# Kernel tuning notes

Hardware: AMD Instinct MI355X
Metric: run time of the kernel (lower is better)

The kernel has to match this reference:

```python
import math
import jax, jax.numpy as jnp
import numpy as np

SIN_DIM = 8
HEADS = 4
HID = 64
EMBED = 6 + 1 + 3 * SIN_DIM + 5 + 2  # 38


def _sinusoidal(v):
    # v: [N] -> [N, SIN_DIM], interleaved sin/cos as in torch.stack(...).flatten(-2)
    div = jnp.exp(jnp.arange(0, SIN_DIM, 2, dtype=jnp.float32) * (-math.log(10000.0) / SIN_DIM))
    scaled = v[:, None] * div  # [N, SIN_DIM//2]
    return jnp.stack([jnp.sin(scaled), jnp.cos(scaled)], axis=-1).reshape(v.shape[0], SIN_DIM)


def _feature_embed(x):
    nt = jnp.clip(x[:, 0].astype(jnp.int32), 0, 5)
    role = jnp.clip(x[:, 5].astype(jnp.int32), 0, 4)
    return jnp.concatenate([
        jax.nn.one_hot(nt, 6, dtype=x.dtype),
        jnp.log1p(x[:, 1])[:, None],
        _sinusoidal(x[:, 2]),
        _sinusoidal(x[:, 3]),
        _sinusoidal(x[:, 4] * 100.0),
        jax.nn.one_hot(role, 5, dtype=x.dtype),
        x[:, 6:7],
        x[:, 7:8],
    ], axis=-1)  # [N, 38]


def _gat(x, adj, W, a_src, a_dst, concat):
    N = x.shape[0]
    h = (x @ W).reshape(N, HEADS, HID)                       # [N,H,D]
    src = jnp.einsum('nhd,hd->nh', h, a_src)                 # [N,H]
    dst = jnp.einsum('nhd,hd->nh', h, a_dst)                 # [N,H]
    e = src[:, None, :] + dst[None, :, :]                    # [N,N,H]
    e = jnp.where(e > 0, e, 0.2 * e)                         # leaky_relu(0.2)
    e = jnp.where(adj[:, :, None] > 0, e, -jnp.inf)
    a = jax.nn.softmax(e, axis=1)                            # softmax over neighbors j
    out = jnp.einsum('njh,nhd->nhd'.replace('nj', 'ij').replace('nhd,', 'jhd,').replace('->nhd', '->ihd'), a, h) if False else jnp.einsum('ijh,jhd->ihd', a, h)
    if concat:
        return out.reshape(N, HEADS * HID)
    return out.mean(axis=1)


def _layernorm(x, g, b, eps=1e-5):
    mu = x.mean(axis=-1, keepdims=True)
    var = ((x - mu) ** 2).mean(axis=-1, keepdims=True)
    return (x - mu) / jnp.sqrt(var + eps) * g + b


def setup_inputs() -> dict:
    key = jax.random.key(0)
    ks = jax.random.split(key, 16)
    N, C = 4096, 512
    # raw node features per FeatureEmbedding docstring
    nt = jax.random.randint(ks[0], (N,), 0, 6).astype(jnp.float32)
    arity = jax.random.randint(ks[1], (N,), 0, 5).astype(jnp.float32)
    arg_pos = jax.random.randint(ks[2], (N,), 0, 8).astype(jnp.float32)
    depth = jax.random.randint(ks[3], (N,), 0, 12).astype(jnp.float32)
    age = jax.random.uniform(ks[4], (N,))
    role = jax.random.randint(ks[5], (N,), 0, 5).astype(jnp.float32)
    pol = jax.random.bernoulli(ks[6], 0.5, (N,)).astype(jnp.float32)
    eq = jax.random.bernoulli(ks[7], 0.2, (N,)).astype(jnp.float32)
    node_features = jnp.stack([nt, arity, arg_pos, depth, age, role, pol, eq], axis=-1)
    adj = (jax.random.uniform(ks[8], (N, N)) < 0.01).astype(jnp.float32)
    adj = jnp.maximum(adj, jnp.eye(N, dtype=jnp.float32))  # self-loops
    pm = (jax.random.uniform(ks[9], (C, N)) < (8.0 / N)).astype(jnp.float32)
    pool_matrix = pm / jnp.clip(pm.sum(axis=1, keepdims=True), 1.0, None)
    def xavier(k, shape):
        fan = shape[0] + shape[-1]
        return jax.random.normal(k, shape, dtype=jnp.float32) * math.sqrt(2.0 / fan)
    return {
        'node_features': node_features, 'adj': adj, 'pool_matrix': pool_matrix,
        'W1': xavier(ks[10], (EMBED, HID * HEADS)),
        'a_src1': xavier(ks[11], (HEADS, HID)), 'a_dst1': xavier(ks[12], (HEADS, HID)),
        'g1': jnp.ones((HID * HEADS,), jnp.float32), 'b1': jnp.zeros((HID * HEADS,), jnp.float32),
        'W2': xavier(ks[13], (HID * HEADS, HID * HEADS)),
        'a_src2': xavier(ks[14], (HEADS, HID)), 'a_dst2': xavier(ks[15], (HEADS, HID)),
        'g2': jnp.ones((HID,), jnp.float32), 'b2': jnp.zeros((HID,), jnp.float32),
        'Ws': xavier(jax.random.fold_in(key, 100), (HID, HID)), 'bs': jnp.zeros((HID,), jnp.float32),
        'Wo': xavier(jax.random.fold_in(key, 101), (HID, 1)), 'bo': jnp.zeros((1,), jnp.float32),
    }


def reference(node_features, adj, pool_matrix, W1, a_src1, a_dst1, g1, b1,
              W2, a_src2, a_dst2, g2, b2, Ws, bs, Wo, bo):
    x = _feature_embed(node_features)                         # [N, 38]
    # layer 1: concat heads -> [N, 256]
    x = jax.nn.elu(_layernorm(_gat(x, adj, W1, a_src1, a_dst1, True), g1, b1))
    # layer 2: mean over heads -> [N, 64]  (dropout is eval-mode no-op)
    x = jax.nn.elu(_layernorm(_gat(x, adj, W2, a_src2, a_dst2, False), g2, b2))
    clause_emb = pool_matrix @ x                               # [C, 64]
    h = jax.nn.relu(clause_emb @ Ws + bs)                      # MLP scorer
    return (h @ Wo + bo)[:, 0]                                 # [C]
```

## Files before the change

### kernel.cpp

```cpp
#include <hip/hip_runtime.h>
#include <math.h>

#define N 4096
#define C 512
#define EMB 38
#define HEADS 4
#define HID 64
#define F1 256
#define MAXN 128
#define R2 8

__device__ __forceinline__ float wr_sum(float v) {
#pragma unroll
    for (int o = 32; o > 0; o >>= 1) v += __shfl_xor(v, o);
    return v;
}
__device__ __forceinline__ float wr_max(float v) {
#pragma unroll
    for (int o = 32; o > 0; o >>= 1) v = fmaxf(v, __shfl_xor(v, o));
    return v;
}

__global__ __launch_bounds__(256) void k_build(const float* __restrict__ adj,
                                               int* __restrict__ cnt, int* __restrict__ idx) {
    int wv = threadIdx.x >> 6, lane = threadIdx.x & 63;
    int i = blockIdx.x * 4 + wv;
    const float4* row = (const float4*)(adj + (size_t)i * N);
    unsigned long long below = (lane == 63) ? ~0ull >> 1 : (1ull << lane) - 1;
    int base = 0;
    int* orow = idx + i * MAXN;
#pragma unroll 2
    for (int it = 0; it < 16; ++it) {
        float4 a = row[it * 64 + lane];
        int col0 = 4 * (it * 64 + lane);
        float vals[4] = {a.x, a.y, a.z, a.w};
#pragma unroll
        for (int comp = 0; comp < 4; ++comp) {
            unsigned long long m = __ballot(vals[comp] > 0.f);
            if (vals[comp] > 0.f) {
                int p = base + __popcll(m & below);
                if (p < MAXN) orow[p] = col0 + comp;
            }
            base += __popcll(m);
        }
    }
    if (lane == 0) cnt[i] = min(base, MAXN);
}

__global__ __launch_bounds__(256) void k_gemm1(const float* __restrict__ nf, const float* __restrict__ W1,
                                               const float* __restrict__ asrc, const float* __restrict__ adst,
                                               float* __restrict__ h1, float* __restrict__ s1, float* __restrict__ d1) {
    int n0 = blockIdx.x * R2, tid = threadIdx.x;
    __shared__ float fs[R2][8];
    __shared__ float xs[R2][40];
    if (tid < R2 * 8) fs[tid >> 3][tid & 7] = nf[(size_t)(n0 + (tid >> 3)) * 8 + (tid & 7)];
    if (tid < R2 * 2) xs[tid >> 1][38 + (tid & 1)] = 0.f;
    __syncthreads();
    {
        int r = tid & 7;
        int t = tid >> 3;
        const float* f = fs[r];
        for (int pass = 0; pass < 2; ++pass, t += 32) {
            if (t >= EMB) break;
            float val;
            if (t < 6) { int nt = min(max((int)f[0], 0), 5); val = (t == nt) ? 1.f : 0.f; }
            else if (t == 6) val = log1pf(f[1]);
            else if (t < 31) {
                int q = (t - 7) & 7, s = (t - 7) >> 3, m = q >> 1;
                float base = (s == 0) ? f[2] : (s == 1) ? f[3] : f[4] * 100.f;
                float div = expf((2.f * m) * (-logf(10000.f) / 8.f));
                float sc = base * div;
                val = (q & 1) ? cosf(sc) : sinf(sc);
            }
            else if (t < 36) { int role = min(max((int)f[5], 0), 4); val = (t - 31 == role) ? 1.f : 0.f; }
            else val = (t == 36) ? f[6] : f[7];
            xs[r][t] = val;
        }
    }
    __syncthreads();
    float acc[R2];
#pragma unroll
    for (int r = 0; r < R2; ++r) acc[r] = 0.f;
#pragma unroll
    for (int kk = 0; kk < 9; ++kk) {
        float w0 = W1[(4 * kk + 0) * F1 + tid];
        float w1 = W1[(4 * kk + 1) * F1 + tid];
        float w2 = W1[(4 * kk + 2) * F1 + tid];
        float w3 = W1[(4 * kk + 3) * F1 + tid];
#pragma unroll
        for (int r = 0; r < R2; ++r) {
            float4 x = *(const float4*)&xs[r][4 * kk];
            acc[r] = fmaf(x.x, w0, fmaf(x.y, w1, fmaf(x.z, w2, fmaf(x.w, w3, acc[r]))));
        }
    }
#pragma unroll
    for (int k = 36; k < EMB; ++k) {
        float wv = W1[k * F1 + tid];
#pragma unroll
        for (int r = 0; r < R2; ++r) acc[r] = fmaf(xs[r][k], wv, acc[r]);
    }
    int h = tid >> 6, lane = tid & 63;
    float av = asrc[tid], dv = adst[tid];
#pragma unroll
    for (int r = 0; r < R2; ++r) {
        h1[(size_t)(n0 + r) * F1 + tid] = acc[r];
        float ss = wr_sum(acc[r] * av);
        float dd = wr_sum(acc[r] * dv);
        if (lane == 0) { s1[(n0 + r) * HEADS + h] = ss; d1[(n0 + r) * HEADS + h] = dd; }
    }
}

__global__ __launch_bounds__(256) void k_gemm2(const float* __restrict__ x1, const float* __restrict__ W2,
                                               const float* __restrict__ asrc, const float* __restrict__ adst,
                                               float* __restrict__ h2, float* __restrict__ s2, float* __restrict__ d2) {
    int n0 = blockIdx.x * R2, tid = threadIdx.x;
    __shared__ float4 xs4[R2][F1 / 4];
    {
        int r = tid >> 5, kk = tid & 31;
        const float4* x1v = (const float4*)x1;
        xs4[r][kk]      = x1v[(size_t)(n0 + r) * 64 + kk];
        xs4[r][kk + 32] = x1v[(size_t)(n0 + r) * 64 + kk + 32];
    }
    __syncthreads();
    float acc[R2];
#pragma unroll
    for (int r = 0; r < R2; ++r) acc[r] = 0.f;
    for (int kk = 0; kk < F1 / 4; ++kk) {
        float w0 = W2[(4 * kk + 0) * F1 + tid];
        float w1 = W2[(4 * kk + 1) * F1 + tid];
        float w2 = W2[(4 * kk + 2) * F1 + tid];
        float w3 = W2[(4 * kk + 3) * F1 + tid];
#pragma unroll
        for (int r = 0; r < R2; ++r) {
            float4 x = xs4[r][kk];
            acc[r] = fmaf(x.x, w0, fmaf(x.y, w1, fmaf(x.z, w2, fmaf(x.w, w3, acc[r]))));
        }
    }
    int h = tid >> 6, lane = tid & 63;
    float av = asrc[tid], dv = adst[tid];
#pragma unroll
    for (int r = 0; r < R2; ++r) {
        h2[(size_t)(n0 + r) * F1 + tid] = acc[r];
        float ss = wr_sum(acc[r] * av);
        float dd = wr_sum(acc[r] * dv);
        if (lane == 0) { s2[(n0 + r) * HEADS + h] = ss; d2[(n0 + r) * HEADS + h] = dd; }
    }
}

__global__ __launch_bounds__(256) void k_agg1(const float* __restrict__ h1, const float* __restrict__ s1,
                                              const float* __restrict__ d1, const int* __restrict__ cnt,
                                              const int* __restrict__ idx, const float* __restrict__ g,
                                              const float* __restrict__ b, float* __restrict__ xo) {
    int i = blockIdx.x, tid = threadIdx.x;
    int wv = tid >> 6, lane = tid & 63;
    __shared__ int nbrs[MAXN];
    __shared__ float wts[HEADS][MAXN + 1];
    __shared__ float lsum[HEADS];
    __shared__ float sacc[4][F1];
    __shared__ float red[HEADS];
    int c = cnt[i];
    if (tid < c) nbrs[tid] = idx[i * MAXN + tid];
    __syncthreads();
    if (tid < c) {
        float4 dd = ((const float4*)d1)[nbrs[tid]];
        float4 ss = ((const float4*)s1)[i];
        float e0 = ss.x + dd.x, e1 = ss.y + dd.y, e2 = ss.z + dd.z, e3 = ss.w + dd.w;
        wts[0][tid] = e0 > 0.f ? e0 : 0.2f * e0;
        wts[1][tid] = e1 > 0.f ? e1 : 0.2f * e1;
        wts[2][tid] = e2 > 0.f ? e2 : 0.2f * e2;
        wts[3][tid] = e3 > 0.f ? e3 : 0.2f * e3;
    }
    __syncthreads();
    {
        float m = -INFINITY;
        for (int jj = lane; jj < c; jj += 64) m = fmaxf(m, wts[wv][jj]);
        m = wr_max(m);
        float l = 0.f;
        for (int jj = lane; jj < c; jj += 64) { float t = expf(wts[wv][jj] - m); wts[wv][jj] = t; l += t; }
        l = wr_sum(l);
        if (lane == 0) lsum[wv] = l;
    }
    __syncthreads();
    int hq = lane >> 4;
    const float4* hv = (const float4*)h1;
    float4 acc = {0.f, 0.f, 0.f, 0.f};
    int jj = wv;
    for (; jj + 4 < c; jj += 8) {
        int na = nbrs[jj], nb = nbrs[jj + 4];
        float wa = wts[hq][jj], wb = wts[hq][jj + 4];
        float4 va = hv[(size_t)na * 64 + lane];
        float4 vb = hv[(size_t)nb * 64 + lane];
        acc.x = fmaf(wa, va.x, acc.x); acc.y = fmaf(wa, va.y, acc.y);
        acc.z = fmaf(wa, va.z, acc.z); acc.w = fmaf(wa, va.w, acc.w);
        acc.x = fmaf(wb, vb.x, acc.x); acc.y = fmaf(wb, vb.y, acc.y);
        acc.z = fmaf(wb, vb.z, acc.z); acc.w = fmaf(wb, vb.w, acc.w);
    }
    for (; jj < c; jj += 4) {
        int na = nbrs[jj];
        float wa = wts[hq][jj];
        float4 va = hv[(size_t)na * 64 + lane];
        acc.x = fmaf(wa, va.x, acc.x); acc.y = fmaf(wa, va.y, acc.y);
        acc.z = fmaf(wa, va.z, acc.z); acc.w = fmaf(wa, va.w, acc.w);
    }
    ((float4*)&sacc[wv][0])[lane] = acc;
    __syncthreads();
    int h = tid >> 6;
    float tot = (sacc[0][tid] + sacc[1][tid] + sacc[2][tid] + sacc[3][tid]) / lsum[h];
    float s = wr_sum(tot);
    if (lane == 0) red[h] = s;
    __syncthreads();
    float mu = (red[0] + red[1] + red[2] + red[3]) * (1.f / F1);
    float dvv = tot - mu;
    float s2 = wr_sum(dvv * dvv);
    __syncthreads();
    if (lane == 0) red[h] = s2;
    __syncthreads();
    float var = (red[0] + red[1] + red[2] + red[3]) * (1.f / F1);
    float y = dvv * rsqrtf(var + 1e-5f) * g[tid] + b[tid];
    xo[(size_t)i * F1 + tid] = y > 0.f ? y : expm1f(y);
}

__global__ __launch_bounds__(256) void k_agg2(const float* __restrict__ h2, const float* __restrict__ s2,
                                              const float* __restrict__ d2, const int* __restrict__ cnt,
                                              const int* __restrict__ idx, const float* __restrict__ g,
                                              const float* __restrict__ b, float* __restrict__ xo) {
    int i = blockIdx.x, tid = threadIdx.x;
    int wv = tid >> 6, lane = tid & 63;
    __shared__ int nbrs[MAXN];
    __shared__ float wts[HEADS][MAXN + 1];
    __shared__ float lsum[HEADS];
    __shared__ float sacc[4][F1];
    int c = cnt[i];
    if (tid < c) nbrs[tid] = idx[i * MAXN + tid];
    __syncthreads();
    if (tid < c) {
        float4 dd = ((const float4*)d2)[nbrs[tid]];
        float4 ss = ((const float4*)s2)[i];
        float e0 = ss.x + dd.x, e1 = ss.y + dd.y, e2 = ss.z + dd.z, e3 = ss.w + dd.w;
        wts[0][tid] = e0 > 0.f ? e0 : 0.2f * e0;
        wts[1][tid] = e1 > 0.f ? e1 : 0.2f * e1;
        wts[2][tid] = e2 > 0.f ? e2 : 0.2f * e2;
        wts[3][tid] = e3 > 0.f ? e3 : 0.2f * e3;
    }
    __syncthreads();
    {
        float m = -INFINITY;
        for (int jj = lane; jj < c; jj += 64) m = fmaxf(m, wts[wv][jj]);
        m = wr_max(m);
        float l = 0.f;
        for (int jj = lane; jj < c; jj += 64) { float t = expf(wts[wv][jj] - m); wts[wv][jj] = t; l += t; }
        l = wr_sum(l);
        if (lane == 0) lsum[wv] = l;
    }
    __syncthreads();
    int hq = lane >> 4;
    const float4* hvv = (const float4*)h2;
    float4 acc = {0.f, 0.f, 0.f, 0.f};
    int jj = wv;
    for (; jj + 4 < c; jj += 8) {
        int na = nbrs[jj], nb = nbrs[jj + 4];
        float wa = wts[hq][jj], wb = wts[hq][jj + 4];
        float4 va = hvv[(size_t)na * 64 + lane];
        float4 vb = hvv[(size_t)nb * 64 + lane];
        acc.x = fmaf(wa, va.x, acc.x); acc.y = fmaf(wa, va.y, acc.y);
        acc.z = fmaf(wa, va.z, acc.z); acc.w = fmaf(wa, va.w, acc.w);
        acc.x = fmaf(wb, vb.x, acc.x); acc.y = fmaf(wb, vb.y, acc.y);
        acc.z = fmaf(wb, vb.z, acc.z); acc.w = fmaf(wb, vb.w, acc.w);
    }
    for (; jj < c; jj += 4) {
        int na = nbrs[jj];
        float wa = wts[hq][jj];
        float4 va = hvv[(size_t)na * 64 + lane];
        acc.x = fmaf(wa, va.x, acc.x); acc.y = fmaf(wa, va.y, acc.y);
        acc.z = fmaf(wa, va.z, acc.z); acc.w = fmaf(wa, va.w, acc.w);
    }
    ((float4*)&sacc[wv][0])[lane] = acc;
    __syncthreads();
    if (wv == 0) {
        float t0 = 0.f, t1 = 0.f, t2 = 0.f, t3 = 0.f;
#pragma unroll
        for (int w = 0; w < 4; ++w) {
            t0 += sacc[w][lane];
            t1 += sacc[w][lane + 64];
            t2 += sacc[w][lane + 128];
            t3 += sacc[w][lane + 192];
        }
        float mv = (t0 / lsum[0] + t1 / lsum[1] + t2 / lsum[2] + t3 / lsum[3]) * 0.25f;
        float mu = wr_sum(mv) * (1.f / HID);
        float dvv = mv - mu;
        float var = wr_sum(dvv * dvv) * (1.f / HID);
        float y = dvv * rsqrtf(var + 1e-5f) * g[lane] + b[lane];
        xo[i * HID + lane] = y > 0.f ? y : expm1f(y);
    }
}

__global__ __launch_bounds__(256) void k_poolscore(const float* __restrict__ pm, const float* __restrict__ x2,
                                                   const float* __restrict__ Ws, const float* __restrict__ bs,
                                                   const float* __restrict__ Wo, const float* __restrict__ bo,
                                                   float* __restrict__ out) {
    int c = blockIdx.x, tid = threadIdx.x;
    int w = tid >> 6, lane = tid & 63;
    __shared__ float sacc[4][HID];
    __shared__ float ce_s[HID];
    float acc = 0.f;
    const float4* pmv = (const float4*)(pm + (size_t)c * N);
#pragma unroll
    for (int it = 0; it < 4; ++it) {
        int vi = w * 256 + it * 64 + lane;
        float4 p4 = pmv[vi];
        float pc[4] = {p4.x, p4.y, p4.z, p4.w};
#pragma unroll
        for (int comp = 0; comp < 4; ++comp) {
            unsigned long long msk = __ballot(pc[comp] != 0.f);
            while (msk) {
                int bpos = __ffsll(msk) - 1;
                msk &= msk - 1;
                float pj = __shfl(pc[comp], bpos);
                int j = (w * 256 + it * 64 + bpos) * 4 + comp;
                acc += pj * x2[(size_t)j * HID + lane];
            }
        }
    }
    sacc[w][lane] = acc;
    __syncthreads();
    if (w == 0) {
        ce_s[lane] = sacc[0][lane] + sacc[1][lane] + sacc[2][lane] + sacc[3][lane];
    }
    __syncthreads();
    if (w == 0) {
        float hd = bs[lane];
#pragma unroll 8
        for (int k = 0; k < HID; ++k) hd = fmaf(ce_s[k], Ws[k * HID + lane], hd);
        hd = fmaxf(hd, 0.f);
        float v = wr_sum(hd * Wo[lane]);
        if (lane == 0) out[c] = v + bo[0];
    }
}

extern "C" void kernel_launch(void* const* d_in, const int* in_sizes, int n_in,
                              void* d_out, int out_size, void* d_ws, size_t ws_size,
                              hipStream_t stream) {
    const float* nf  = (const float*)d_in[0];
    const float* adj = (const float*)d_in[1];
    const float* pm  = (const float*)d_in[2];
    const float* W1  = (const float*)d_in[3];
    const float* as1 = (const float*)d_in[4];
    const float* ad1 = (const float*)d_in[5];
    const float* g1  = (const float*)d_in[6];
    const float* b1  = (const float*)d_in[7];
    const float* W2  = (const float*)d_in[8];
    const float* as2 = (const float*)d_in[9];
    const float* ad2 = (const float*)d_in[10];
    const float* g2  = (const float*)d_in[11];
    const float* b2  = (const float*)d_in[12];
    const float* Ws  = (const float*)d_in[13];
    const float* bs  = (const float*)d_in[14];
    const float* Wo  = (const float*)d_in[15];
    const float* bo  = (const float*)d_in[16];
    float* out = (float*)d_out;

    float* p = (float*)d_ws;
    float* h1  = p; p += (size_t)N * F1;
    float* s1  = p; p += (size_t)N * HEADS;
    float* d1  = p; p += (size_t)N * HEADS;
    float* x1  = p; p += (size_t)N * F1;
    float* h2  = p; p += (size_t)N * F1;
    float* s2  = p; p += (size_t)N * HEADS;
    float* d2  = p; p += (size_t)N * HEADS;
    float* x2  = p; p += (size_t)N * HID;
    int* cnt = (int*)p;
    int* idx = cnt + N;

    k_build<<<N / 4, 256, 0, stream>>>(adj, cnt, idx);
    k_gemm1<<<N / R2, 256, 0, stream>>>(nf, W1, as1, ad1, h1, s1, d1);
    k_agg1<<<N, 256, 0, stream>>>(h1, s1, d1, cnt, idx, g1, b1, x1);
    k_gemm2<<<N / R2, 256, 0, stream>>>(x1, W2, as2, ad2, h2, s2, d2);
    k_agg2<<<N, 256, 0, stream>>>(h2, s2, d2, cnt, idx, g2, b2, x2);
    k_poolscore<<<C, 256, 0, stream>>>(pm, x2, Ws, bs, Wo, bo, out);
}
```

Baseline: 201.5 us.

## Fuse all GAT stages into one cooperative persistent kernel with grid syncs

Replaces the six separate launches with a single cooperative kernel of 512 blocks that runs adjacency compaction, both GEMMs, both aggregations and pooling/scoring, separated by grid-wide barriers. Each block handles 8 rows per stage, and shared memory is reused across stages through a union. The aim is to remove per-kernel launch and drain overhead. In exchange, the aggregation stages drop from 4096 blocks to 512 blocks looping serially, which may reduce latency hiding, and the grid syncs add their own cost. The old multi-kernel path is kept as a fallback if the cooperative launch fails.

```diff
diff --git a/kernel.cpp b/kernel.cpp
--- a/kernel.cpp
+++ b/kernel.cpp
@@ -1,5 +1,8 @@
 #include <hip/hip_runtime.h>
+#include <hip/hip_cooperative_groups.h>
 #include <math.h>
+
+namespace cg = cooperative_groups;
 
 #define N 4096
 #define C 512
@@ -8,7 +11,8 @@
 #define HID 64
 #define F1 256
 #define MAXN 128
-#define R2 8
+#define RPB 8
+#define BLKS 512
 
 __device__ __forceinline__ float wr_sum(float v) {
 #pragma unroll
@@ -21,7 +25,344 @@
     return v;
 }
 
-__global__ __launch_bounds__(256) void k_build(const float* __restrict__ adj,
+struct SmemAgg {
+    int nbrs[MAXN];
+    float wts[HEADS][MAXN + 1];
+    float lsum[HEADS];
+    float sacc[4][F1];
+    float red[HEADS];
+};
+struct SmemG1 {
+    float fs[RPB][8];
+    float xs[RPB][40];
+};
+struct SmemG2 {
+    float4 xs4[RPB][F1 / 4];
+};
+struct SmemPool {
+    float sacc[4][HID];
+    float ce[HID];
+};
+union Smem {
+    SmemAgg a;
+    SmemG1 g1;
+    SmemG2 g2;
+    SmemPool p;
+};
+
+__global__ __launch_bounds__(256, 2) void k_all(
+        const float* __restrict__ adj, const float* __restrict__ nf, const float* __restrict__ pm,
+        const float* __restrict__ W1, const float* __restrict__ as1, const float* __restrict__ ad1,
+        const float* __restrict__ g1, const float* __restrict__ b1,
+        const float* __restrict__ W2, const float* __restrict__ as2, const float* __restrict__ ad2,
+        const float* __restrict__ g2, const float* __restrict__ b2,
+        const float* __restrict__ Wsc, const float* __restrict__ bsc,
+        const float* __restrict__ Wo, const float* __restrict__ bo,
+        float* __restrict__ out, float* __restrict__ ws) {
+    cg::grid_group gg = cg::this_grid();
+    __shared__ Smem sm;
+    int tid = threadIdx.x, blk = blockIdx.x;
+    int wv = tid >> 6, lane = tid & 63;
+
+    float* h1 = ws;
+    float* s1 = h1 + (size_t)N * F1;
+    float* d1 = s1 + N * HEADS;
+    float* x1 = d1 + N * HEADS;
+    float* h2 = x1 + (size_t)N * F1;
+    float* s2 = h2 + (size_t)N * F1;
+    float* d2 = s2 + N * HEADS;
+    float* x2 = d2 + N * HEADS;
+    int* cnt  = (int*)(x2 + N * HID);
+    int* idx  = cnt + N;
+
+#pragma unroll
+    for (int rep = 0; rep < 2; ++rep) {
+        int i = blk * RPB + rep * 4 + wv;
+        const float4* row = (const float4*)(adj + (size_t)i * N);
+        unsigned long long below = (lane == 63) ? (~0ull >> 1) : ((1ull << lane) - 1);
+        int base = 0;
+        int* orow = idx + i * MAXN;
+        for (int it = 0; it < 16; ++it) {
+            float4 a = row[it * 64 + lane];
+            int col0 = 4 * (it * 64 + lane);
+            float vals[4] = {a.x, a.y, a.z, a.w};
+#pragma unroll
+            for (int comp = 0; comp < 4; ++comp) {
+                unsigned long long m = __ballot(vals[comp] > 0.f);
+                if (vals[comp] > 0.f) {
+                    int p = base + __popcll(m & below);
+                    if (p < MAXN) orow[p] = col0 + comp;
+                }
+                base += __popcll(m);
+            }
+        }
+        if (lane == 0) cnt[i] = min(base, MAXN);
+    }
+
+    {
+        int n0 = blk * RPB;
+        if (tid < RPB * 8) sm.g1.fs[tid >> 3][tid & 7] = nf[(size_t)n0 * 8 + tid];
+        if (tid < RPB * 2) sm.g1.xs[tid >> 1][38 + (tid & 1)] = 0.f;
+        __syncthreads();
+        {
+            int r = tid & 7;
+            int t = tid >> 3;
+            const float* f = sm.g1.fs[r];
+            for (int pass = 0; pass < 2; ++pass, t += 32) {
+                if (t >= EMB) break;
+                float val;
+                if (t < 6) { int nt = min(max((int)f[0], 0), 5); val = (t == nt) ? 1.f : 0.f; }
+                else if (t == 6) val = log1pf(f[1]);
+                else if (t < 31) {
+                    int q = (t - 7) & 7, s = (t - 7) >> 3, m = q >> 1;
+                    float base = (s == 0) ? f[2] : (s == 1) ? f[3] : f[4] * 100.f;
+                    float div = expf((2.f * m) * (-logf(10000.f) / 8.f));
+                    float sc = base * div;
+                    val = (q & 1) ? cosf(sc) : sinf(sc);
+                }
+                else if (t < 36) { int role = min(max((int)f[5], 0), 4); val = (t - 31 == role) ? 1.f : 0.f; }
+                else val = (t == 36) ? f[6] : f[7];
+                sm.g1.xs[r][t] = val;
+            }
+        }
+        __syncthreads();
+        float acc[RPB];
+#pragma unroll
+        for (int r = 0; r < RPB; ++r) acc[r] = 0.f;
+#pragma unroll
+        for (int kk = 0; kk < 9; ++kk) {
+            float w0 = W1[(4 * kk + 0) * F1 + tid];
+            float w1 = W1[(4 * kk + 1) * F1 + tid];
+            float w2 = W1[(4 * kk + 2) * F1 + tid];
+            float w3 = W1[(4 * kk + 3) * F1 + tid];
+#pragma unroll
+            for (int r = 0; r < RPB; ++r) {
+                float4 x = *(const float4*)&sm.g1.xs[r][4 * kk];
+                acc[r] = fmaf(x.x, w0, fmaf(x.y, w1, fmaf(x.z, w2, fmaf(x.w, w3, acc[r]))));
+            }
+        }
+#pragma unroll
+        for (int k = 36; k < EMB; ++k) {
+            float wvv = W1[k * F1 + tid];
+#pragma unroll
+            for (int r = 0; r < RPB; ++r) acc[r] = fmaf(sm.g1.xs[r][k], wvv, acc[r]);
+        }
+        float av = as1[tid], dvv = ad1[tid];
+#pragma unroll
+        for (int r = 0; r < RPB; ++r) {
+            h1[(size_t)(n0 + r) * F1 + tid] = acc[r];
+            float ssum = wr_sum(acc[r] * av);
+            float dsum = wr_sum(acc[r] * dvv);
+            if (lane == 0) { s1[(n0 + r) * HEADS + wv] = ssum; d1[(n0 + r) * HEADS + wv] = dsum; }
+        }
+    }
+    gg.sync();
+
+    for (int rr = 0; rr < RPB; ++rr) {
+        int i = blk * RPB + rr;
+        __syncthreads();
+        int c = cnt[i];
+        if (tid < c) sm.a.nbrs[tid] = idx[i * MAXN + tid];
+        __syncthreads();
+        if (tid < c) {
+            float4 dd = ((const float4*)d1)[sm.a.nbrs[tid]];
+            float4 ss = ((const float4*)s1)[i];
+            float e0 = ss.x + dd.x, e1 = ss.y + dd.y, e2 = ss.z + dd.z, e3 = ss.w + dd.w;
+            sm.a.wts[0][tid] = e0 > 0.f ? e0 : 0.2f * e0;
+            sm.a.wts[1][tid] = e1 > 0.f ? e1 : 0.2f * e1;
+            sm.a.wts[2][tid] = e2 > 0.f ? e2 : 0.2f * e2;
+            sm.a.wts[3][tid] = e3 > 0.f ? e3 : 0.2f * e3;
+        }
+        __syncthreads();
+        {
+            float m = -INFINITY;
+            for (int jj = lane; jj < c; jj += 64) m = fmaxf(m, sm.a.wts[wv][jj]);
+            m = wr_max(m);
+            float l = 0.f;
+            for (int jj = lane; jj < c; jj += 64) { float t = expf(sm.a.wts[wv][jj] - m); sm.a.wts[wv][jj] = t; l += t; }
+            l = wr_sum(l);
+            if (lane == 0) sm.a.lsum[wv] = l;
+        }
+        __syncthreads();
+        int hq = lane >> 4;
+        const float4* hv = (const float4*)h1;
+        float4 acc = {0.f, 0.f, 0.f, 0.f};
+        int jj = wv;
+        for (; jj + 4 < c; jj += 8) {
+            int na = sm.a.nbrs[jj], nb = sm.a.nbrs[jj + 4];
+            float wa = sm.a.wts[hq][jj], wb = sm.a.wts[hq][jj + 4];
+            float4 va = hv[(size_t)na * 64 + lane];
+            float4 vb = hv[(size_t)nb * 64 + lane];
+            acc.x = fmaf(wa, va.x, acc.x); acc.y = fmaf(wa, va.y, acc.y);
+            acc.z = fmaf(wa, va.z, acc.z); acc.w = fmaf(wa, va.w, acc.w);
+            acc.x = fmaf(wb, vb.x, acc.x); acc.y = fmaf(wb, vb.y, acc.y);
+            acc.z = fmaf(wb, vb.z, acc.z); acc.w = fmaf(wb, vb.w, acc.w);
+        }
+        for (; jj < c; jj += 4) {
+            int na = sm.a.nbrs[jj];
+            float wa = sm.a.wts[hq][jj];
+            float4 va = hv[(size_t)na * 64 + lane];
+            acc.x = fmaf(wa, va.x, acc.x); acc.y = fmaf(wa, va.y, acc.y);
+            acc.z = fmaf(wa, va.z, acc.z); acc.w = fmaf(wa, va.w, acc.w);
+        }
+        ((float4*)&sm.a.sacc[wv][0])[lane] = acc;
+        __syncthreads();
+        float tot = (sm.a.sacc[0][tid] + sm.a.sacc[1][tid] + sm.a.sacc[2][tid] + sm.a.sacc[3][tid]) / sm.a.lsum[wv];
+        float s = wr_sum(tot);
+        if (lane == 0) sm.a.red[wv] = s;
+        __syncthreads();
+        float mu = (sm.a.red[0] + sm.a.red[1] + sm.a.red[2] + sm.a.red[3]) * (1.f / F1);
+        float dvv = tot - mu;
+        float s2v = wr_sum(dvv * dvv);
+        __syncthreads();
+        if (lane == 0) sm.a.red[wv] = s2v;
+        __syncthreads();
+        float var = (sm.a.red[0] + sm.a.red[1] + sm.a.red[2] + sm.a.red[3]) * (1.f / F1);
+        float y = dvv * rsqrtf(var + 1e-5f) * g1[tid] + b1[tid];
+        x1[(size_t)i * F1 + tid] = y > 0.f ? y : expm1f(y);
+    }
+
+    {
+        __syncthreads();
+        int n0 = blk * RPB;
+        {
+            int r = tid >> 5, kk = tid & 31;
+            const float4* x1v = (const float4*)x1;
+            sm.g2.xs4[r][kk]      = x1v[(size_t)(n0 + r) * 64 + kk];
+            sm.g2.xs4[r][kk + 32] = x1v[(size_t)(n0 + r) * 64 + kk + 32];
+        }
+        __syncthreads();
+        float acc[RPB];
+#pragma unroll
+        for (int r = 0; r < RPB; ++r) acc[r] = 0.f;
+        for (int kk = 0; kk < F1 / 4; ++kk) {
+            float w0 = W2[(4 * kk + 0) * F1 + tid];
+            float w1 = W2[(4 * kk + 1) * F1 + tid];
+            float w2 = W2[(4 * kk + 2) * F1 + tid];
+            float w3 = W2[(4 * kk + 3) * F1 + tid];
+#pragma unroll
+            for (int r = 0; r < RPB; ++r) {
+                float4 x = sm.g2.xs4[r][kk];
+                acc[r] = fmaf(x.x, w0, fmaf(x.y, w1, fmaf(x.z, w2, fmaf(x.w, w3, acc[r]))));
+            }
+        }
+        float av = as2[tid], dvv = ad2[tid];
+#pragma unroll
+        for (int r = 0; r < RPB; ++r) {
+            h2[(size_t)(n0 + r) * F1 + tid] = acc[r];
+            float ssum = wr_sum(acc[r] * av);
+            float dsum = wr_sum(acc[r] * dvv);
+            if (lane == 0) { s2[(n0 + r) * HEADS + wv] = ssum; d2[(n0 + r) * HEADS + wv] = dsum; }
+        }
+    }
+    gg.sync();
+
+    for (int rr = 0; rr < RPB; ++rr) {
+        int i = blk * RPB + rr;
+        __syncthreads();
+        int c = cnt[i];
+        if (tid < c) sm.a.nbrs[tid] = idx[i * MAXN + tid];
+        __syncthreads();
+        if (tid < c) {
+            float4 dd = ((const float4*)d2)[sm.a.nbrs[tid]];
+            float4 ss = ((const float4*)s2)[i];
+            float e0 = ss.x + dd.x, e1 = ss.y + dd.y, e2 = ss.z + dd.z, e3 = ss.w + dd.w;
+            sm.a.wts[0][tid] = e0 > 0.f ? e0 : 0.2f * e0;
+            sm.a.wts[1][tid] = e1 > 0.f ? e1 : 0.2f * e1;
+            sm.a.wts[2][tid] = e2 > 0.f ? e2 : 0.2f * e2;
+            sm.a.wts[3][tid] = e3 > 0.f ? e3 : 0.2f * e3;
+        }
+        __syncthreads();
+        {
+            float m = -INFINITY;
+            for (int jj = lane; jj < c; jj += 64) m = fmaxf(m, sm.a.wts[wv][jj]);
+            m = wr_max(m);
+            float l = 0.f;
+            for (int jj = lane; jj < c; jj += 64) { float t = expf(sm.a.wts[wv][jj] - m); sm.a.wts[wv][jj] = t; l += t; }
+            l = wr_sum(l);
+            if (lane == 0) sm.a.lsum[wv] = l;
+        }
+        __syncthreads();
+        int hq = lane >> 4;
+        const float4* hvv = (const float4*)h2;
+        float4 acc = {0.f, 0.f, 0.f, 0.f};
+        int jj = wv;
+        for (; jj + 4 < c; jj += 8) {
+            int na = sm.a.nbrs[jj], nb = sm.a.nbrs[jj + 4];
+            float wa = sm.a.wts[hq][jj], wb = sm.a.wts[hq][jj + 4];
+            float4 va = hvv[(size_t)na * 64 + lane];
+            float4 vb = hvv[(size_t)nb * 64 + lane];
+            acc.x = fmaf(wa, va.x, acc.x); acc.y = fmaf(wa, va.y, acc.y);
+            acc.z = fmaf(wa, va.z, acc.z); acc.w = fmaf(wa, va.w, acc.w);
+            acc.x = fmaf(wb, vb.x, acc.x); acc.y = fmaf(wb, vb.y, acc.y);
+            acc.z = fmaf(wb, vb.z, acc.z); acc.w = fmaf(wb, vb.w, acc.w);
+        }
+        for (; jj < c; jj += 4) {
+            int na = sm.a.nbrs[jj];
+            float wa = sm.a.wts[hq][jj];
+            float4 va = hvv[(size_t)na * 64 + lane];
+            acc.x = fmaf(wa, va.x, acc.x); acc.y = fmaf(wa, va.y, acc.y);
+            acc.z = fmaf(wa, va.z, acc.z); acc.w = fmaf(wa, va.w, acc.w);
+        }
+        ((float4*)&sm.a.sacc[wv][0])[lane] = acc;
+        __syncthreads();
+        if (wv == 0) {
+            float t0 = 0.f, t1 = 0.f, t2 = 0.f, t3 = 0.f;
+#pragma unroll
+            for (int w = 0; w < 4; ++w) {
+                t0 += sm.a.sacc[w][lane];
+                t1 += sm.a.sacc[w][lane + 64];
+                t2 += sm.a.sacc[w][lane + 128];
+                t3 += sm.a.sacc[w][lane + 192];
+            }
+            float mv = (t0 / sm.a.lsum[0] + t1 / sm.a.lsum[1] + t2 / sm.a.lsum[2] + t3 / sm.a.lsum[3]) * 0.25f;
+            float mu = wr_sum(mv) * (1.f / HID);
+            float dvv = mv - mu;
+            float var = wr_sum(dvv * dvv) * (1.f / HID);
+            float y = dvv * rsqrtf(var + 1e-5f) * g2[lane] + b2[lane];
+            x2[i * HID + lane] = y > 0.f ? y : expm1f(y);
+        }
+        __syncthreads();
+    }
+    gg.sync();
+
+    {
+        int cc = blk;
+        float acc = 0.f;
+        const float4* pmv = (const float4*)(pm + (size_t)cc * N);
+#pragma unroll
+        for (int it = 0; it < 4; ++it) {
+            int vi = wv * 256 + it * 64 + lane;
+            float4 p4 = pmv[vi];
+            float pc[4] = {p4.x, p4.y, p4.z, p4.w};
+#pragma unroll
+            for (int comp = 0; comp < 4; ++comp) {
+                unsigned long long msk = __ballot(pc[comp] != 0.f);
+                while (msk) {
+                    int bpos = __ffsll(msk) - 1;
+                    msk &= msk - 1;
+                    float pj = __shfl(pc[comp], bpos);
+                    int j = (wv * 256 + it * 64 + bpos) * 4 + comp;
+                    acc += pj * x2[(size_t)j * HID + lane];
+                }
+            }
+        }
+        sm.p.sacc[wv][lane] = acc;
+        __syncthreads();
+        if (wv == 0) sm.p.ce[lane] = sm.p.sacc[0][lane] + sm.p.sacc[1][lane] + sm.p.sacc[2][lane] + sm.p.sacc[3][lane];
+        __syncthreads();
+        if (wv == 0) {
+            float hd = bsc[lane];
+#pragma unroll 8
+            for (int k = 0; k < HID; ++k) hd = fmaf(sm.p.ce[k], Wsc[k * HID + lane], hd);
+            hd = fmaxf(hd, 0.f);
+            float v = wr_sum(hd * Wo[lane]);
+            if (lane == 0) out[cc] = v + bo[0];
+        }
+    }
+}
+
+__global__ __launch_bounds__(256) void f_build(const float* __restrict__ adj,
                                                int* __restrict__ cnt, int* __restrict__ idx) {
     int wv = threadIdx.x >> 6, lane = threadIdx.x & 63;
     int i = blockIdx.x * 4 + wv;
@@ -47,14 +388,14 @@
     if (lane == 0) cnt[i] = min(base, MAXN);
 }
 
-__global__ __launch_bounds__(256) void k_gemm1(const float* __restrict__ nf, const float* __restrict__ W1,
+__global__ __launch_bounds__(256) void f_gemm1(const float* __restrict__ nf, const float* __restrict__ W1,
                                                const float* __restrict__ asrc, const float* __restrict__ adst,
                                                float* __restrict__ h1, float* __restrict__ s1, float* __restrict__ d1) {
-    int n0 = blockIdx.x * R2, tid = threadIdx.x;
-    __shared__ float fs[R2][8];
-    __shared__ float xs[R2][40];
-    if (tid < R2 * 8) fs[tid >> 3][tid & 7] = nf[(size_t)(n0 + (tid >> 3)) * 8 + (tid & 7)];
-    if (tid < R2 * 2) xs[tid >> 1][38 + (tid & 1)] = 0.f;
+    int n0 = blockIdx.x * RPB, tid = threadIdx.x;
+    __shared__ float fs[RPB][8];
+    __shared__ float xs[RPB][40];
+    if (tid < RPB * 8) fs[tid >> 3][tid & 7] = nf[(size_t)n0 * 8 + tid];
+    if (tid < RPB * 2) xs[tid >> 1][38 + (tid & 1)] = 0.f;
     __syncthreads();
     {
         int r = tid & 7;
@@ -78,9 +419,9 @@
         }
     }
     __syncthreads();
-    float acc[R2];
-#pragma unroll
-    for (int r = 0; r < R2; ++r) acc[r] = 0.f;
+    float acc[RPB];
+#pragma unroll
+    for (int r = 0; r < RPB; ++r) acc[r] = 0.f;
 #pragma unroll
     for (int kk = 0; kk < 9; ++kk) {
         float w0 = W1[(4 * kk + 0) * F1 + tid];
@@ -88,21 +429,21 @@
         float w2 = W1[(4 * kk + 2) * F1 + tid];
         float w3 = W1[(4 * kk + 3) * F1 + tid];
 #pragma unroll
-        for (int r = 0; r < R2; ++r) {
+        for (int r = 0; r < RPB; ++r) {
             float4 x = *(const float4*)&xs[r][4 * kk];
             acc[r] = fmaf(x.x, w0, fmaf(x.y, w1, fmaf(x.z, w2, fmaf(x.w, w3, acc[r]))));
         }
     }
 #pragma unroll
     for (int k = 36; k < EMB; ++k) {
-        float wv = W1[k * F1 + tid];
-#pragma unroll
-        for (int r = 0; r < R2; ++r) acc[r] = fmaf(xs[r][k], wv, acc[r]);
+        float wvv = W1[k * F1 + tid];
+#pragma unroll
+        for (int r = 0; r < RPB; ++r) acc[r] = fmaf(xs[r][k], wvv, acc[r]);
     }
     int h = tid >> 6, lane = tid & 63;
     float av = asrc[tid], dv = adst[tid];
 #pragma unroll
-    for (int r = 0; r < R2; ++r) {
+    for (int r = 0; r < RPB; ++r) {
         h1[(size_t)(n0 + r) * F1 + tid] = acc[r];
         float ss = wr_sum(acc[r] * av);
         float dd = wr_sum(acc[r] * dv);
@@ -110,11 +451,11 @@
     }
 }
 
-__global__ __launch_bounds__(256) void k_gemm2(const float* __restrict__ x1, const float* __restrict__ W2,
+__global__ __launch_bounds__(256) void f_gemm2(const float* __restrict__ x1, const float* __restrict__ W2,
                                                const float* __restrict__ asrc, const float* __restrict__ adst,
                                                float* __restrict__ h2, float* __restrict__ s2, float* __restrict__ d2) {
-    int n0 = blockIdx.x * R2, tid = threadIdx.x;
-    __shared__ float4 xs4[R2][F1 / 4];
+    int n0 = blockIdx.x * RPB, tid = threadIdx.x;
+    __shared__ float4 xs4[RPB][F1 / 4];
     {
         int r = tid >> 5, kk = tid & 31;
         const float4* x1v = (const float4*)x1;
@@ -122,16 +463,16 @@
         xs4[r][kk + 32] = x1v[(size_t)(n0 + r) * 64 + kk + 32];
     }
     __syncthreads();
-    float acc[R2];
-#pragma unroll
-    for (int r = 0; r < R2; ++r) acc[r] = 0.f;
+    float acc[RPB];
+#pragma unroll
+    for (int r = 0; r < RPB; ++r) acc[r] = 0.f;
     for (int kk = 0; kk < F1 / 4; ++kk) {
         float w0 = W2[(4 * kk + 0) * F1 + tid];
         float w1 = W2[(4 * kk + 1) * F1 + tid];
         float w2 = W2[(4 * kk + 2) * F1 + tid];
         float w3 = W2[(4 * kk + 3) * F1 + tid];
 #pragma unroll
-        for (int r = 0; r < R2; ++r) {
+        for (int r = 0; r < RPB; ++r) {
             float4 x = xs4[r][kk];
             acc[r] = fmaf(x.x, w0, fmaf(x.y, w1, fmaf(x.z, w2, fmaf(x.w, w3, acc[r]))));
         }
@@ -139,7 +480,7 @@
     int h = tid >> 6, lane = tid & 63;
     float av = asrc[tid], dv = adst[tid];
 #pragma unroll
-    for (int r = 0; r < R2; ++r) {
+    for (int r = 0; r < RPB; ++r) {
         h2[(size_t)(n0 + r) * F1 + tid] = acc[r];
         float ss = wr_sum(acc[r] * av);
         float dd = wr_sum(acc[r] * dv);
@@ -147,7 +488,7 @@
     }
 }
 
-__global__ __launch_bounds__(256) void k_agg1(const float* __restrict__ h1, const float* __restrict__ s1,
+__global__ __launch_bounds__(256) void f_agg1(const float* __restrict__ h1, const float* __restrict__ s1,
                                               const float* __restrict__ d1, const int* __restrict__ cnt,
                                               const int* __restrict__ idx, const float* __restrict__ g,
                                               const float* __restrict__ b, float* __restrict__ xo) {
@@ -204,23 +545,22 @@
     }
     ((float4*)&sacc[wv][0])[lane] = acc;
     __syncthreads();
-    int h = tid >> 6;
-    float tot = (sacc[0][tid] + sacc[1][tid] + sacc[2][tid] + sacc[3][tid]) / lsum[h];
+    float tot = (sacc[0][tid] + sacc[1][tid] + sacc[2][tid] + sacc[3][tid]) / lsum[wv];
     float s = wr_sum(tot);
-    if (lane == 0) red[h] = s;
+    if (lane == 0) red[wv] = s;
     __syncthreads();
     float mu = (red[0] + red[1] + red[2] + red[3]) * (1.f / F1);
     float dvv = tot - mu;
     float s2 = wr_sum(dvv * dvv);
     __syncthreads();
-    if (lane == 0) red[h] = s2;
+    if (lane == 0) red[wv] = s2;
     __syncthreads();
     float var = (red[0] + red[1] + red[2] + red[3]) * (1.f / F1);
     float y = dvv * rsqrtf(var + 1e-5f) * g[tid] + b[tid];
     xo[(size_t)i * F1 + tid] = y > 0.f ? y : expm1f(y);
 }
 
-__global__ __launch_bounds__(256) void k_agg2(const float* __restrict__ h2, const float* __restrict__ s2,
+__global__ __launch_bounds__(256) void f_agg2(const float* __restrict__ h2, const float* __restrict__ s2,
                                               const float* __restrict__ d2, const int* __restrict__ cnt,
                                               const int* __restrict__ idx, const float* __restrict__ g,
                                               const float* __restrict__ b, float* __restrict__ xo) {
@@ -294,7 +634,7 @@
     }
 }
 
-__global__ __launch_bounds__(256) void k_poolscore(const float* __restrict__ pm, const float* __restrict__ x2,
+__global__ __launch_bounds__(256) void f_poolscore(const float* __restrict__ pm, const float* __restrict__ x2,
                                                    const float* __restrict__ Ws, const float* __restrict__ bs,
                                                    const float* __restrict__ Wo, const float* __restrict__ bo,
                                                    float* __restrict__ out) {
@@ -323,9 +663,7 @@
     }
     sacc[w][lane] = acc;
     __syncthreads();
-    if (w == 0) {
-        ce_s[lane] = sacc[0][lane] + sacc[1][lane] + sacc[2][lane] + sacc[3][lane];
-    }
+    if (w == 0) ce_s[lane] = sacc[0][lane] + sacc[1][lane] + sacc[2][lane] + sacc[3][lane];
     __syncthreads();
     if (w == 0) {
         float hd = bs[lane];
@@ -353,13 +691,14 @@
     const float* ad2 = (const float*)d_in[10];
     const float* g2  = (const float*)d_in[11];
     const float* b2  = (const float*)d_in[12];
-    const float* Ws  = (const float*)d_in[13];
-    const float* bs  = (const float*)d_in[14];
+    const float* Wsc = (const float*)d_in[13];
+    const float* bsc = (const float*)d_in[14];
     const float* Wo  = (const float*)d_in[15];
     const float* bo  = (const float*)d_in[16];
-    float* out = (float*)d_out;
-
-    float* p = (float*)d_ws;
+    float* outp = (float*)d_out;
+    float* wsp  = (float*)d_ws;
+
+    float* p = wsp;
     float* h1  = p; p += (size_t)N * F1;
     float* s1  = p; p += (size_t)N * HEADS;
     float* d1  = p; p += (size_t)N * HEADS;
@@ -371,10 +710,17 @@
     int* cnt = (int*)p;
     int* idx = cnt + N;
 
-    k_build<<<N / 4, 256, 0, stream>>>(adj, cnt, idx);
-    k_gemm1<<<N / R2, 256, 0, stream>>>(nf, W1, as1, ad1, h1, s1, d1);
-    k_agg1<<<N, 256, 0, stream>>>(h1, s1, d1, cnt, idx, g1, b1, x1);
-    k_gemm2<<<N / R2, 256, 0, stream>>>(x1, W2, as2, ad2, h2, s2, d2);
-    k_agg2<<<N, 256, 0, stream>>>(h2, s2, d2, cnt, idx, g2, b2, x2);
-    k_poolscore<<<C, 256, 0, stream>>>(pm, x2, Ws, bs, Wo, bo, out);
-}
+    void* args[] = {(void*)&adj, (void*)&nf, (void*)&pm, (void*)&W1, (void*)&as1, (void*)&ad1,
+                    (void*)&g1, (void*)&b1, (void*)&W2, (void*)&as2, (void*)&ad2, (void*)&g2,
+                    (void*)&b2, (void*)&Wsc, (void*)&bsc, (void*)&Wo, (void*)&bo,
+                    (void*)&outp, (void*)&wsp};
+    hipError_t err = hipLaunchCooperativeKernel(k_all, dim3(BLKS), dim3(256), args, 0, stream);
+    if (err != hipSuccess) {
+        f_build<<<N / 4, 256, 0, stream>>>(adj, cnt, idx);
+        f_gemm1<<<N / RPB, 256, 0, stream>>>(nf, W1, as1, ad1, h1, s1, d1);
+        f_agg1<<<N, 256, 0, stream>>>(h1, s1, d1, cnt, idx, g1, b1, x1);
+        f_gemm2<<<N / RPB, 256, 0, stream>>>(x1, W2, as2, ad2, h2, s2, d2);
+        f_agg2<<<N, 256, 0, stream>>>(h2, s2, d2, cnt, idx, g2, b2, x2);
+        f_poolscore<<<C, 256, 0, stream>>>(pm, x2, Wsc, bsc, Wo, bo, outp);
+    }
+}
```

Result: slower. 470.4 us (+133.4%).

## Merge adjacency build and layer-1 GEMM into one launch; unroll neighbor gathers

Applied to the files above, without the earlier changes.

Combines the adjacency-list build kernel and the layer-1 feature-embed GEMM into a single launch. Block indices pick the role, so the two independent jobs run concurrently and one launch is saved. The build loop now software-prefetches the next adjacency float4, and both aggregation kernels unroll the neighbor gather to four outstanding loads per iteration for more memory-level parallelism. This costs more register pressure, and the added launch-bounds occupancy hint may constrain register allocation.

```diff
diff --git a/kernel.cpp b/kernel.cpp
--- a/kernel.cpp
+++ b/kernel.cpp
@@ -8,7 +8,8 @@
 #define HID 64
 #define F1 256
 #define MAXN 128
-#define R2 8
+#define RPB 8
+#define BUILD_BLKS (N / 4)
 
 __device__ __forceinline__ float wr_sum(float v) {
 #pragma unroll
@@ -21,40 +22,43 @@
     return v;
 }
 
-__global__ __launch_bounds__(256) void k_build(const float* __restrict__ adj,
-                                               int* __restrict__ cnt, int* __restrict__ idx) {
-    int wv = threadIdx.x >> 6, lane = threadIdx.x & 63;
-    int i = blockIdx.x * 4 + wv;
-    const float4* row = (const float4*)(adj + (size_t)i * N);
-    unsigned long long below = (lane == 63) ? ~0ull >> 1 : (1ull << lane) - 1;
-    int base = 0;
-    int* orow = idx + i * MAXN;
-#pragma unroll 2
-    for (int it = 0; it < 16; ++it) {
-        float4 a = row[it * 64 + lane];
-        int col0 = 4 * (it * 64 + lane);
-        float vals[4] = {a.x, a.y, a.z, a.w};
-#pragma unroll
-        for (int comp = 0; comp < 4; ++comp) {
-            unsigned long long m = __ballot(vals[comp] > 0.f);
-            if (vals[comp] > 0.f) {
-                int p = base + __popcll(m & below);
-                if (p < MAXN) orow[p] = col0 + comp;
-            }
-            base += __popcll(m);
-        }
-    }
-    if (lane == 0) cnt[i] = min(base, MAXN);
-}
-
-__global__ __launch_bounds__(256) void k_gemm1(const float* __restrict__ nf, const float* __restrict__ W1,
+__global__ __launch_bounds__(256, 4) void k_bg(const float* __restrict__ adj,
+                                               int* __restrict__ cnt, int* __restrict__ idx,
+                                               const float* __restrict__ nf, const float* __restrict__ W1,
                                                const float* __restrict__ asrc, const float* __restrict__ adst,
                                                float* __restrict__ h1, float* __restrict__ s1, float* __restrict__ d1) {
-    int n0 = blockIdx.x * R2, tid = threadIdx.x;
-    __shared__ float fs[R2][8];
-    __shared__ float xs[R2][40];
-    if (tid < R2 * 8) fs[tid >> 3][tid & 7] = nf[(size_t)(n0 + (tid >> 3)) * 8 + (tid & 7)];
-    if (tid < R2 * 2) xs[tid >> 1][38 + (tid & 1)] = 0.f;
+    int tid = threadIdx.x;
+    int wv = tid >> 6, lane = tid & 63;
+    if (blockIdx.x < BUILD_BLKS) {
+        int i = blockIdx.x * 4 + wv;
+        const float4* row = (const float4*)(adj + (size_t)i * N);
+        unsigned long long below = (lane == 63) ? (~0ull >> 1) : ((1ull << lane) - 1);
+        int base = 0;
+        int* orow = idx + i * MAXN;
+        float4 nxt = row[lane];
+        for (int it = 0; it < 16; ++it) {
+            float4 a = nxt;
+            if (it < 15) nxt = row[(it + 1) * 64 + lane];
+            int col0 = 4 * (it * 64 + lane);
+            float vals[4] = {a.x, a.y, a.z, a.w};
+#pragma unroll
+            for (int comp = 0; comp < 4; ++comp) {
+                unsigned long long m = __ballot(vals[comp] > 0.f);
+                if (vals[comp] > 0.f) {
+                    int p = base + __popcll(m & below);
+                    if (p < MAXN) orow[p] = col0 + comp;
+                }
+                base += __popcll(m);
+            }
+        }
+        if (lane == 0) cnt[i] = min(base, MAXN);
+        return;
+    }
+    int n0 = (blockIdx.x - BUILD_BLKS) * RPB;
+    __shared__ float fs[RPB][8];
+    __shared__ float xs[RPB][40];
+    if (tid < RPB * 8) fs[tid >> 3][tid & 7] = nf[(size_t)n0 * 8 + tid];
+    if (tid < RPB * 2) xs[tid >> 1][38 + (tid & 1)] = 0.f;
     __syncthreads();
     {
         int r = tid & 7;
@@ -78,9 +82,9 @@
         }
     }
     __syncthreads();
-    float acc[R2];
-#pragma unroll
-    for (int r = 0; r < R2; ++r) acc[r] = 0.f;
+    float acc[RPB];
+#pragma unroll
+    for (int r = 0; r < RPB; ++r) acc[r] = 0.f;
 #pragma unroll
     for (int kk = 0; kk < 9; ++kk) {
         float w0 = W1[(4 * kk + 0) * F1 + tid];
@@ -88,33 +92,32 @@
         float w2 = W1[(4 * kk + 2) * F1 + tid];
         float w3 = W1[(4 * kk + 3) * F1 + tid];
 #pragma unroll
-        for (int r = 0; r < R2; ++r) {
+        for (int r = 0; r < RPB; ++r) {
             float4 x = *(const float4*)&xs[r][4 * kk];
             acc[r] = fmaf(x.x, w0, fmaf(x.y, w1, fmaf(x.z, w2, fmaf(x.w, w3, acc[r]))));
         }
     }
 #pragma unroll
     for (int k = 36; k < EMB; ++k) {
-        float wv = W1[k * F1 + tid];
-#pragma unroll
-        for (int r = 0; r < R2; ++r) acc[r] = fmaf(xs[r][k], wv, acc[r]);
-    }
-    int h = tid >> 6, lane = tid & 63;
+        float wvv = W1[k * F1 + tid];
+#pragma unroll
+        for (int r = 0; r < RPB; ++r) acc[r] = fmaf(xs[r][k], wvv, acc[r]);
+    }
     float av = asrc[tid], dv = adst[tid];
 #pragma unroll
-    for (int r = 0; r < R2; ++r) {
+    for (int r = 0; r < RPB; ++r) {
         h1[(size_t)(n0 + r) * F1 + tid] = acc[r];
         float ss = wr_sum(acc[r] * av);
         float dd = wr_sum(acc[r] * dv);
-        if (lane == 0) { s1[(n0 + r) * HEADS + h] = ss; d1[(n0 + r) * HEADS + h] = dd; }
+        if (lane == 0) { s1[(n0 + r) * HEADS + wv] = ss; d1[(n0 + r) * HEADS + wv] = dd; }
     }
 }
 
 __global__ __launch_bounds__(256) void k_gemm2(const float* __restrict__ x1, const float* __restrict__ W2,
                                                const float* __restrict__ asrc, const float* __restrict__ adst,
                                                float* __restrict__ h2, float* __restrict__ s2, float* __restrict__ d2) {
-    int n0 = blockIdx.x * R2, tid = threadIdx.x;
-    __shared__ float4 xs4[R2][F1 / 4];
+    int n0 = blockIdx.x * RPB, tid = threadIdx.x;
+    __shared__ float4 xs4[RPB][F1 / 4];
     {
         int r = tid >> 5, kk = tid & 31;
         const float4* x1v = (const float4*)x1;
@@ -122,16 +125,16 @@
         xs4[r][kk + 32] = x1v[(size_t)(n0 + r) * 64 + kk + 32];
     }
     __syncthreads();
-    float acc[R2];
-#pragma unroll
-    for (int r = 0; r < R2; ++r) acc[r] = 0.f;
+    float acc[RPB];
+#pragma unroll
+    for (int r = 0; r < RPB; ++r) acc[r] = 0.f;
     for (int kk = 0; kk < F1 / 4; ++kk) {
         float w0 = W2[(4 * kk + 0) * F1 + tid];
         float w1 = W2[(4 * kk + 1) * F1 + tid];
         float w2 = W2[(4 * kk + 2) * F1 + tid];
         float w3 = W2[(4 * kk + 3) * F1 + tid];
 #pragma unroll
-        for (int r = 0; r < R2; ++r) {
+        for (int r = 0; r < RPB; ++r) {
             float4 x = xs4[r][kk];
             acc[r] = fmaf(x.x, w0, fmaf(x.y, w1, fmaf(x.z, w2, fmaf(x.w, w3, acc[r]))));
         }
@@ -139,7 +142,7 @@
     int h = tid >> 6, lane = tid & 63;
     float av = asrc[tid], dv = adst[tid];
 #pragma unroll
-    for (int r = 0; r < R2; ++r) {
+    for (int r = 0; r < RPB; ++r) {
         h2[(size_t)(n0 + r) * F1 + tid] = acc[r];
         float ss = wr_sum(acc[r] * av);
         float dd = wr_sum(acc[r] * dv);
@@ -185,15 +188,21 @@
     const float4* hv = (const float4*)h1;
     float4 acc = {0.f, 0.f, 0.f, 0.f};
     int jj = wv;
-    for (; jj + 4 < c; jj += 8) {
-        int na = nbrs[jj], nb = nbrs[jj + 4];
-        float wa = wts[hq][jj], wb = wts[hq][jj + 4];
+    for (; jj + 12 < c; jj += 16) {
+        int na = nbrs[jj], nb = nbrs[jj + 4], nc = nbrs[jj + 8], nd = nbrs[jj + 12];
+        float wa = wts[hq][jj], wb = wts[hq][jj + 4], wc = wts[hq][jj + 8], wd = wts[hq][jj + 12];
         float4 va = hv[(size_t)na * 64 + lane];
         float4 vb = hv[(size_t)nb * 64 + lane];
+        float4 vc = hv[(size_t)nc * 64 + lane];
+        float4 vd = hv[(size_t)nd * 64 + lane];
         acc.x = fmaf(wa, va.x, acc.x); acc.y = fmaf(wa, va.y, acc.y);
         acc.z = fmaf(wa, va.z, acc.z); acc.w = fmaf(wa, va.w, acc.w);
         acc.x = fmaf(wb, vb.x, acc.x); acc.y = fmaf(wb, vb.y, acc.y);
         acc.z = fmaf(wb, vb.z, acc.z); acc.w = fmaf(wb, vb.w, acc.w);
+        acc.x = fmaf(wc, vc.x, acc.x); acc.y = fmaf(wc, vc.y, acc.y);
+        acc.z = fmaf(wc, vc.z, acc.z); acc.w = fmaf(wc, vc.w, acc.w);
+        acc.x = fmaf(wd, vd.x, acc.x); acc.y = fmaf(wd, vd.y, acc.y);
+        acc.z = fmaf(wd, vd.z, acc.z); acc.w = fmaf(wd, vd.w, acc.w);
     }
     for (; jj < c; jj += 4) {
         int na = nbrs[jj];
@@ -204,16 +213,15 @@
     }
     ((float4*)&sacc[wv][0])[lane] = acc;
     __syncthreads();
-    int h = tid >> 6;
-    float tot = (sacc[0][tid] + sacc[1][tid] + sacc[2][tid] + sacc[3][tid]) / lsum[h];
+    float tot = (sacc[0][tid] + sacc[1][tid] + sacc[2][tid] + sacc[3][tid]) / lsum[wv];
     float s = wr_sum(tot);
-    if (lane == 0) red[h] = s;
+    if (lane == 0) red[wv] = s;
     __syncthreads();
     float mu = (red[0] + red[1] + red[2] + red[3]) * (1.f / F1);
     float dvv = tot - mu;
     float s2 = wr_sum(dvv * dvv);
     __syncthreads();
-    if (lane == 0) red[h] = s2;
+    if (lane == 0) red[wv] = s2;
     __syncthreads();
     float var = (red[0] + red[1] + red[2] + red[3]) * (1.f / F1);
     float y = dvv * rsqrtf(var + 1e-5f) * g[tid] + b[tid];
@@ -257,15 +265,21 @@
     const float4* hvv = (const float4*)h2;
     float4 acc = {0.f, 0.f, 0.f, 0.f};
     int jj = wv;
-    for (; jj + 4 < c; jj += 8) {
-        int na = nbrs[jj], nb = nbrs[jj + 4];
-        float wa = wts[hq][jj], wb = wts[hq][jj + 4];
+    for (; jj + 12 < c; jj += 16) {
+        int na = nbrs[jj], nb = nbrs[jj + 4], nc = nbrs[jj + 8], nd = nbrs[jj + 12];
+        float wa = wts[hq][jj], wb = wts[hq][jj + 4], wc = wts[hq][jj + 8], wd = wts[hq][jj + 12];
         float4 va = hvv[(size_t)na * 64 + lane];
         float4 vb = hvv[(size_t)nb * 64 + lane];
+        float4 vc = hvv[(size_t)nc * 64 + lane];
+        float4 vd = hvv[(size_t)nd * 64 + lane];
         acc.x = fmaf(wa, va.x, acc.x); acc.y = fmaf(wa, va.y, acc.y);
         acc.z = fmaf(wa, va.z, acc.z); acc.w = fmaf(wa, va.w, acc.w);
         acc.x = fmaf(wb, vb.x, acc.x); acc.y = fmaf(wb, vb.y, acc.y);
         acc.z = fmaf(wb, vb.z, acc.z); acc.w = fmaf(wb, vb.w, acc.w);
+        acc.x = fmaf(wc, vc.x, acc.x); acc.y = fmaf(wc, vc.y, acc.y);
+        acc.z = fmaf(wc, vc.z, acc.z); acc.w = fmaf(wc, vc.w, acc.w);
+        acc.x = fmaf(wd, vd.x, acc.x); acc.y = fmaf(wd, vd.y, acc.y);
+        acc.z = fmaf(wd, vd.z, acc.z); acc.w = fmaf(wd, vd.w, acc.w);
     }
     for (; jj < c; jj += 4) {
         int na = nbrs[jj];
@@ -323,9 +337,7 @@
     }
     sacc[w][lane] = acc;
     __syncthreads();
-    if (w == 0) {
-        ce_s[lane] = sacc[0][lane] + sacc[1][lane] + sacc[2][lane] + sacc[3][lane];
-    }
+    if (w == 0) ce_s[lane] = sacc[0][lane] + sacc[1][lane] + sacc[2][lane] + sacc[3][lane];
     __syncthreads();
     if (w == 0) {
         float hd = bs[lane];
@@ -371,10 +383,9 @@
     int* cnt = (int*)p;
     int* idx = cnt + N;
 
-    k_build<<<N / 4, 256, 0, stream>>>(adj, cnt, idx);
-    k_gemm1<<<N / R2, 256, 0, stream>>>(nf, W1, as1, ad1, h1, s1, d1);
+    k_bg<<<BUILD_BLKS + N / RPB, 256, 0, stream>>>(adj, cnt, idx, nf, W1, as1, ad1, h1, s1, d1);
     k_agg1<<<N, 256, 0, stream>>>(h1, s1, d1, cnt, idx, g1, b1, x1);
-    k_gemm2<<<N / R2, 256, 0, stream>>>(x1, W2, as2, ad2, h2, s2, d2);
+    k_gemm2<<<N / RPB, 256, 0, stream>>>(x1, W2, as2, ad2, h2, s2, d2);
     k_agg2<<<N, 256, 0, stream>>>(h2, s2, d2, cnt, idx, g2, b2, x2);
     k_poolscore<<<C, 256, 0, stream>>>(pm, x2, Ws, bs, Wo, bo, out);
 }
```

New measurement: 253.6 us. +25.8%, slower.
